# Performance work log

Measured on AMD Instinct MI355X. Metric: run time of the kernel, lower is better.

The kernel has to match this reference:

```python
import jax, jax.numpy as jnp
import numpy as np

H = 16        # num_heads
D = 64        # head_dim
HID = 1024    # hidden_size
WIN = 256     # window_size
GLOBAL = 0    # single global token index {0}


def _rope_tables(L):
    inv_freq = 1.0 / (10000.0 ** (jnp.arange(0, D, 2, dtype=jnp.float32) / D))
    pos = jnp.arange(L, dtype=jnp.float32)
    freqs = pos[:, None] * inv_freq[None, :]          # [L, D/2]
    emb = jnp.concatenate([freqs, freqs], axis=-1)     # [L, D]
    return jnp.cos(emb), jnp.sin(emb)


def _apply_rope(x, cos, sin):
    # x: [B, H, L, D]; cos/sin: [L, D]
    x1, x2 = x[..., : D // 2], x[..., D // 2 :]
    rot = jnp.concatenate([-x2, x1], axis=-1)
    return x * cos[None, None] + rot * sin[None, None]


def setup_inputs() -> dict:
    key = jax.random.key(0)
    ks = jax.random.split(key, 6)
    B, L = 2, 2048
    s = 0.02
    return {
        "hidden_states": jax.random.normal(ks[0], (B, L, HID), jnp.float32),
        "q_w": jax.random.normal(ks[1], (HID, HID), jnp.float32) * s,
        "q_b": jnp.zeros((HID,), jnp.float32),
        "k_w": jax.random.normal(ks[2], (HID, HID), jnp.float32) * s,
        "k_b": jnp.zeros((HID,), jnp.float32),
        "v_w": jax.random.normal(ks[3], (HID, HID), jnp.float32) * s,
        "v_b": jnp.zeros((HID,), jnp.float32),
        "o_w": jax.random.normal(ks[4], (HID, HID), jnp.float32) * s,
        "o_b": jnp.zeros((HID,), jnp.float32),
    }


def reference(hidden_states, q_w, q_b, k_w, k_b, v_w, v_b, o_w, o_b):
    B, L, _ = hidden_states.shape
    # torch Linear: y = x @ W^T + b
    q = hidden_states @ q_w.T + q_b
    k = hidden_states @ k_w.T + k_b
    v = hidden_states @ v_w.T + v_b
    # [B, L, H*D] -> [B, H, L, D]
    q = q.reshape(B, L, H, D).transpose(0, 2, 1, 3)
    k = k.reshape(B, L, H, D).transpose(0, 2, 1, 3)
    v = v.reshape(B, L, H, D).transpose(0, 2, 1, 3)

    cos, sin = _rope_tables(L)
    q = _apply_rope(q, cos, sin)
    k = _apply_rope(k, cos, sin)

    scale = jnp.float32(np.sqrt(D))
    scores = jnp.einsum("bhid,bhjd->bhij", q, k) / scale  # [B, H, L, L]

    # sparse mask: causal AND (within sliding window OR global token)
    i = jnp.arange(L)[:, None]
    j = jnp.arange(L)[None, :]
    keep = (j <= i) & (((i - j) < WIN) | (j == GLOBAL))    # [L, L] bool
    scores = jnp.where(keep[None, None], scores, jnp.float32(-jnp.inf))

    probs = jax.nn.softmax(scores, axis=-1)
    out = jnp.einsum("bhij,bhjd->bhid", probs, v)           # [B, H, L, D]
    out = out.transpose(0, 2, 1, 3).reshape(B, L, HID)
    return out @ o_w.T + o_b
```

## Files before the change

kernel.cpp:

```cpp
#include <hip/hip_runtime.h>
#include <hip/hip_bf16.h>
#include <cstdint>

#define LSEQ   2048
#define HID    1024
#define WIN    256
#define MROWS  4096

typedef unsigned short u16;
typedef unsigned int   u32;
typedef __attribute__((ext_vector_type(8))) short bf16x8;
typedef __attribute__((ext_vector_type(4))) float f32x4;
typedef __attribute__((address_space(1))) const unsigned int as1_uint;
typedef __attribute__((address_space(3))) unsigned int as3_uint;
typedef __attribute__((address_space(3))) char as3_char;

static __device__ __forceinline__ float bf2f(u16 u) {
  union { u32 u; float f; } c; c.u = ((u32)u) << 16; return c.f;
}
static __device__ __forceinline__ u16 f2bf(float f) {
  union { float f; u32 u; } c; c.f = f;
  u32 r = c.u + 0x7fffu + ((c.u >> 16) & 1u);
  return (u16)(r >> 16);
}

__global__ void cvt_all(const float* __restrict__ hidden,
                        const float* __restrict__ qw, const float* __restrict__ kw,
                        const float* __restrict__ vw, const float* __restrict__ ow,
                        u16* __restrict__ hbf, u16* __restrict__ wbf,
                        float* __restrict__ tab) {
  const int b = blockIdx.x;
  if (b >= 8192) {
    const int idx = (b - 8192) * 256 + threadIdx.x;
    const int l = idx >> 5, d = idx & 31;
    float invf = exp2f(-(float)d * (13.287712379549449f / 32.0f));
    float ang = (float)l * invf;
    tab[l * 64 + d]      = cosf(ang);
    tab[l * 64 + 32 + d] = sinf(ang);
    return;
  }
  const int i = b * 256 + threadIdx.x;
  const float* src; u16* dst; int off;
  if (i < (1 << 20)) {
    src = hidden; dst = hbf; off = i;
  } else {
    const int j = i - (1 << 20);
    const int seg = j >> 18;
    off = j & ((1 << 18) - 1);
    src = (seg == 0) ? qw : (seg == 1) ? kw : (seg == 2) ? vw : ow;
    dst = wbf + ((size_t)seg << 20);
  }
  float4 v = ((const float4*)src)[off];
  u32 lo = (u32)f2bf(v.x) | ((u32)f2bf(v.y) << 16);
  u32 hi = (u32)f2bf(v.z) | ((u32)f2bf(v.w) << 16);
  ((uint2*)dst)[off] = make_uint2(lo, hi);
}

template<int NW>
__global__ __launch_bounds__(256, 2) void gemm_bt(
    const u16* __restrict__ A, const u16* __restrict__ W,
    const float* __restrict__ b0, const float* __restrict__ b1, const float* __restrict__ b2,
    u16* __restrict__ outb, float* __restrict__ outf, const float* __restrict__ tab,
    u16* __restrict__ vt)
{
  __shared__ u16 As[128 * 32];
  __shared__ u16 Bs[128 * 32];
  const int tid = threadIdx.x;
  const int lane = tid & 63, w = tid >> 6;
  const int wr = w >> 1, wc = w & 1;

  const int GX = (NW == 3) ? 24 : 8;
  const int CH = (GX * 32) >> 3;
  int fid = blockIdx.y * GX + blockIdx.x;
  fid = (fid & 7) * CH + (fid >> 3);
  const int bx = fid % GX, by = fid / GX;

  const char* gA = (const char*)(A + (size_t)(by*128 + w*32 + (lane >> 2)) * HID) + (lane & 3) * 16;
  const char* gB = (const char*)(W + (size_t)(bx*128 + w*32 + (lane >> 2)) * HID) + (lane & 3) * 16;
  as3_char* lA = (as3_char*)As + w * 2048;
  as3_char* lB = (as3_char*)Bs + w * 2048;

  f32x4 acc[4][4] = {};

  for (int kt = 0; kt < HID; kt += 32) {
    __syncthreads();
    __builtin_amdgcn_global_load_lds((as1_uint*)(gA + kt*2),         (as3_uint*)lA,          16, 0, 0);
    __builtin_amdgcn_global_load_lds((as1_uint*)(gA + kt*2 + 32768), (as3_uint*)(lA + 1024), 16, 0, 0);
    __builtin_amdgcn_global_load_lds((as1_uint*)(gB + kt*2),         (as3_uint*)lB,          16, 0, 0);
    __builtin_amdgcn_global_load_lds((as1_uint*)(gB + kt*2 + 32768), (as3_uint*)(lB + 1024), 16, 0, 0);
    __syncthreads();

    const int kq = (lane >> 4) * 8;
    bf16x8 af[4], bfr[4];
    #pragma unroll
    for (int mm = 0; mm < 4; ++mm)
      af[mm] = *(const bf16x8*)&As[(wr*64 + mm*16 + (lane & 15)) * 32 + kq];
    #pragma unroll
    for (int nn = 0; nn < 4; ++nn)
      bfr[nn] = *(const bf16x8*)&Bs[(wc*64 + nn*16 + (lane & 15)) * 32 + kq];
    #pragma unroll
    for (int mm = 0; mm < 4; ++mm)
      #pragma unroll
      for (int nn = 0; nn < 4; ++nn)
        acc[mm][nn] = __builtin_amdgcn_mfma_f32_16x16x32_bf16(af[mm], bfr[nn], acc[mm][nn], 0, 0, 0);
  }

  const int which = (NW == 3) ? (bx >> 3) : 0;
  const float* bp = (NW == 3) ? (which == 0 ? b0 : (which == 1 ? b1 : b2)) : b0;
  const int cb = (NW == 3) ? ((bx & 7) * 128) : bx * 128;
  u16* ob_ = (NW == 3) ? (outb + (size_t)which * MROWS * HID) : (u16*)nullptr;
  const int rowg = by * 128 + wr * 64;
  const int c = lane & 15, g = lane >> 4;

  #pragma unroll
  for (int nn = 0; nn < 4; ++nn) {
    const float bias = bp[cb + wc * 64 + nn * 16 + c];
    #pragma unroll
    for (int mm = 0; mm < 4; ++mm)
      #pragma unroll
      for (int r = 0; r < 4; ++r) acc[mm][nn][r] += bias;
  }

  if (NW == 3 && which < 2) {
    const float QS = (which == 0) ? (0.125f * 1.4426950408889634f) : 1.0f;
    #pragma unroll
    for (int mm = 0; mm < 4; ++mm) {
      #pragma unroll
      for (int r = 0; r < 4; ++r) {
        const int l = (rowg + mm * 16 + (g << 2) + r) & (LSEQ - 1);
        const float* trow = tab + l * 64;
        const float cs0 = trow[c],      sn0 = trow[32 + c];
        const float cs1 = trow[16 + c], sn1 = trow[48 + c];
        const float x0 = acc[mm][0][r], y0 = acc[mm][2][r];
        const float x1 = acc[mm][1][r], y1 = acc[mm][3][r];
        acc[mm][0][r] = (x0 * cs0 - y0 * sn0) * QS;
        acc[mm][2][r] = (y0 * cs0 + x0 * sn0) * QS;
        acc[mm][1][r] = (x1 * cs1 - y1 * sn1) * QS;
        acc[mm][3][r] = (y1 * cs1 + x1 * sn1) * QS;
      }
    }
  }

  if (NW == 3 && which == 2) {
    #pragma unroll
    for (int nn = 0; nn < 4; ++nn) {
      const int cl = cb + wc * 64 + nn * 16 + c;
      const int hh = cl >> 6, hd = cl & 63;
      #pragma unroll
      for (int mm = 0; mm < 4; ++mm) {
        const int rb = rowg + mm * 16 + (g << 2);
        const int b_ = rb >> 11, l = rb & (LSEQ - 1);
        u16 t4[4];
        #pragma unroll
        for (int r = 0; r < 4; ++r) t4[r] = f2bf(acc[mm][nn][r]);
        *(uint2*)&vt[(size_t)((b_ * 16 + hh) * 64 + hd) * LSEQ + l] = *(uint2*)t4;
      }
    }
  } else {
    #pragma unroll
    for (int nn = 0; nn < 4; ++nn) {
      const int cl = cb + wc * 64 + nn * 16 + c;
      #pragma unroll
      for (int mm = 0; mm < 4; ++mm) {
        const int rb = rowg + mm * 16 + (g << 2);
        #pragma unroll
        for (int r = 0; r < 4; ++r) {
          if (NW == 3) ob_[(size_t)(rb + r) * HID + cl] = f2bf(acc[mm][nn][r]);
          else         outf[(size_t)(rb + r) * HID + cl] = acc[mm][nn][r];
        }
      }
    }
  }
}

__global__ __launch_bounds__(256) void attn_mfma(
    const u16* __restrict__ Q, const u16* __restrict__ K,
    const u16* __restrict__ Vt, u16* __restrict__ O)
{
  __shared__ u16 Ks[2 * 64 * 64];
  __shared__ u16 Vs[2 * 64 * 64];
  __shared__ u16 Ps[4 * 16 * 64];

  const int tid = threadIdx.x, lane = tid & 63, w = tid >> 6;
  const int g = lane >> 4, c = lane & 15;
  const int qb = (blockIdx.x & 31) * 64;
  const int bh = blockIdx.x >> 5;
  const int h = bh & 15;
  const size_t row0 = (size_t)(bh >> 4) * LSEQ;
  const int qw = qb + w * 16;

  const int srow = (w << 4) + (lane >> 3);
  const int scol = ((lane & 7) * 16) ^ ((lane >> 3) << 4);
  const char* gKb = (const char*)(K + (row0 + srow) * HID + h * 64) + scol;
  const char* gVb = (const char*)(Vt + (size_t)(bh * 64 + srow) * LSEQ) + scol;

  const u16* qptr = Q + (row0 + qw + c) * HID + h * 64 + g * 8;
  bf16x8 qa0 = *(const bf16x8*)qptr;
  bf16x8 qa1 = *(const bf16x8*)(qptr + 32);

  const int cbk = qb >> 6;
  int cf = (qb - (WIN - 1)) >> 6; if (cf < 0) cf = 0;

  float psum[4] = {0.f, 0.f, 0.f, 0.f};
  f32x4 o_[4];
  #pragma unroll
  for (int dt = 0; dt < 4; ++dt) o_[dt] = f32x4{0.f, 0.f, 0.f, 0.f};

  if (cf > 0) {
    const u16* k0p = K + row0 * HID + h * 64 + g * 8;
    bf16x8 k0a = *(const bf16x8*)k0p;
    bf16x8 k0b = *(const bf16x8*)(k0p + 32);
    float part = 0.f;
    #pragma unroll
    for (int j = 0; j < 8; ++j)
      part += bf2f((u16)qa0[j]) * bf2f((u16)k0a[j]) + bf2f((u16)qa1[j]) * bf2f((u16)k0b[j]);
    part += __shfl_xor(part, 16);
    part += __shfl_xor(part, 32);
    float p0 = exp2f(part);
    float prs[4];
    #pragma unroll
    for (int r = 0; r < 4; ++r) { prs[r] = __shfl(p0, g * 4 + r); psum[r] = prs[r]; }
    #pragma unroll
    for (int dt = 0; dt < 4; ++dt) {
      float v0 = bf2f(Vt[(size_t)(bh * 64 + dt * 16 + c) * LSEQ]);
      #pragma unroll
      for (int r = 0; r < 4; ++r) o_[dt][r] = prs[r] * v0;
    }
  }

  {
    const size_t kadv = (size_t)cf * 64 * 2048;
    const size_t vadv = (size_t)cf * 128;
    as3_char* lk = (as3_char*)Ks + w * 2048;
    as3_char* lv = (as3_char*)Vs + w * 2048;
    __builtin_amdgcn_global_load_lds((as1_uint*)(gKb + kadv),         (as3_uint*)lk,          16, 0, 0);
    __builtin_amdgcn_global_load_lds((as1_uint*)(gKb + kadv + 16384), (as3_uint*)(lk + 1024), 16, 0, 0);
    __builtin_amdgcn_global_load_lds((as1_uint*)(gVb + vadv),         (as3_uint*)lv,          16, 0, 0);
    __builtin_amdgcn_global_load_lds((as1_uint*)(gVb + vadv + 32768), (as3_uint*)(lv + 1024), 16, 0, 0);
  }

  int buf = 0;
  for (int ci = cf; ci <= cbk; ++ci) {
    const int c0 = ci * 64;
    __syncthreads();

    if (ci < cbk) {
      const size_t kadv = (size_t)(c0 + 64) * 2048;
      const size_t vadv = (size_t)(c0 + 64) * 2;
      as3_char* lk = (as3_char*)Ks + (buf ^ 1) * 8192 + w * 2048;
      as3_char* lv = (as3_char*)Vs + (buf ^ 1) * 8192 + w * 2048;
      __builtin_amdgcn_global_load_lds((as1_uint*)(gKb + kadv),         (as3_uint*)lk,          16, 0, 0);
      __builtin_amdgcn_global_load_lds((as1_uint*)(gKb + kadv + 16384), (as3_uint*)(lk + 1024), 16, 0, 0);
      __builtin_amdgcn_global_load_lds((as1_uint*)(gVb + vadv),         (as3_uint*)lv,          16, 0, 0);
      __builtin_amdgcn_global_load_lds((as1_uint*)(gVb + vadv + 32768), (as3_uint*)(lv + 1024), 16, 0, 0);
    }

    const char* ksbase = (const char*)Ks + buf * 8192;
    const char* vsbase = (const char*)Vs + buf * 8192;

    f32x4 st[4];
    #pragma unroll
    for (int t = 0; t < 4; ++t) {
      const int krow = t * 16 + c;
      const char* kbase = ksbase + krow * 128;
      const int sw = (krow & 7) << 4;
      bf16x8 kb0 = *(const bf16x8*)(kbase + ((g * 16) ^ sw));
      bf16x8 kb1 = *(const bf16x8*)(kbase + ((g * 16 + 64) ^ sw));
      st[t] = f32x4{0.f, 0.f, 0.f, 0.f};
      st[t] = __builtin_amdgcn_mfma_f32_16x16x32_bf16(qa0, kb0, st[t], 0, 0, 0);
      st[t] = __builtin_amdgcn_mfma_f32_16x16x32_bf16(qa1, kb1, st[t], 0, 0, 0);
    }

    float e[4][4];
    #pragma unroll
    for (int r = 0; r < 4; ++r) {
      const int qi = qw + g * 4 + r;
      #pragma unroll
      for (int t = 0; t < 4; ++t) {
        const int kj = c0 + t * 16 + c;
        const bool valid = (kj <= qi) && ((qi - kj < WIN) || (kj == 0));
        e[r][t] = valid ? exp2f(st[t][r]) : 0.f;
      }
      psum[r] += (e[r][0] + e[r][1]) + (e[r][2] + e[r][3]);
    }

    char* pwb = (char*)Ps + w * 2048;
    #pragma unroll
    for (int r = 0; r < 4; ++r) {
      const int q = g * 4 + r;
      char* prow = pwb + q * 128;
      const int sw = (q & 7) << 4;
      *(u16*)(prow + (((c + 0)  * 2) ^ sw)) = f2bf(e[r][0]);
      *(u16*)(prow + (((c + 16) * 2) ^ sw)) = f2bf(e[r][1]);
      *(u16*)(prow + (((c + 32) * 2) ^ sw)) = f2bf(e[r][2]);
      *(u16*)(prow + (((c + 48) * 2) ^ sw)) = f2bf(e[r][3]);
    }
    asm volatile("s_waitcnt lgkmcnt(0)" ::: "memory");
    __builtin_amdgcn_sched_barrier(0);

    bf16x8 pa[2];
    #pragma unroll
    for (int kh = 0; kh < 2; ++kh) {
      const int inner = (g * 16 + kh * 64) ^ ((c & 7) << 4);
      pa[kh] = *(const bf16x8*)(pwb + c * 128 + inner);
    }

    #pragma unroll
    for (int dt = 0; dt < 4; ++dt) {
      const int drow = dt * 16 + c;
      const char* vbase = vsbase + drow * 128;
      const int sw = (drow & 7) << 4;
      bf16x8 vb0 = *(const bf16x8*)(vbase + ((g * 16) ^ sw));
      bf16x8 vb1 = *(const bf16x8*)(vbase + ((g * 16 + 64) ^ sw));
      o_[dt] = __builtin_amdgcn_mfma_f32_16x16x32_bf16(pa[0], vb0, o_[dt], 0, 0, 0);
      o_[dt] = __builtin_amdgcn_mfma_f32_16x16x32_bf16(pa[1], vb1, o_[dt], 0, 0, 0);
    }
    buf ^= 1;
  }

  #pragma unroll
  for (int r = 0; r < 4; ++r) {
    #pragma unroll
    for (int off = 1; off < 16; off <<= 1) psum[r] += __shfl_xor(psum[r], off);
  }

  #pragma unroll
  for (int r = 0; r < 4; ++r) {
    const float inv = 1.f / psum[r];
    u16* orow = O + (row0 + qw + g * 4 + r) * HID + h * 64;
    #pragma unroll
    for (int dt = 0; dt < 4; ++dt)
      orow[dt * 16 + c] = f2bf(o_[dt][r] * inv);
  }
}

extern "C" void kernel_launch(void* const* d_in, const int* in_sizes, int n_in,
                              void* d_out, int out_size, void* d_ws, size_t ws_size,
                              hipStream_t stream) {
  const float* hidden = (const float*)d_in[0];
  const float* qw = (const float*)d_in[1];
  const float* qb = (const float*)d_in[2];
  const float* kw = (const float*)d_in[3];
  const float* kb = (const float*)d_in[4];
  const float* vw = (const float*)d_in[5];
  const float* vb = (const float*)d_in[6];
  const float* ow = (const float*)d_in[7];
  const float* ob = (const float*)d_in[8];
  float* out = (float*)d_out;

  u16* hbf = (u16*)d_ws;
  u16* wbf = hbf + (size_t)MROWS * HID;
  u16* qkv = wbf + (size_t)4 * HID * HID;
  float* tab = (float*)(qkv + (size_t)3 * MROWS * HID);
  u16* Vt = (u16*)(tab + (size_t)LSEQ * 64);

  cvt_all<<<8448, 256, 0, stream>>>(hidden, qw, kw, vw, ow, hbf, wbf, tab);

  gemm_bt<3><<<dim3(24, 32), 256, 0, stream>>>(hbf, wbf, qb, kb, vb, qkv, nullptr, tab, Vt);
  attn_mfma<<<1024, 256, 0, stream>>>(qkv, qkv + (size_t)MROWS * HID, Vt, qkv);
  gemm_bt<1><<<dim3(8, 32), 256, 0, stream>>>(qkv, wbf + (size_t)3 * HID * HID,
                                              ob, ob, ob, nullptr, out, nullptr, nullptr);
}
```

Measured before the change: 93.49 us.

## Double GEMM K-tile to 64 with XOR-swizzled LDS and interleaved RoPE table

The bf16 GEMM now stages K=64 per iteration instead of 32, which halves the number of barrier pairs per K loop. The global-to-LDS layout is rewritten as 128-byte rows with an XOR swizzle, and fragment reads apply the same swizzle to avoid LDS bank conflicts. The RoPE cos/sin table is stored interleaved so the epilogue can fetch each pair with one float2 load. LDS use doubles to 32 KB per block, which may limit occupancy at the requested two blocks per CU.

```diff
diff --git a/kernel.cpp b/kernel.cpp
--- a/kernel.cpp
+++ b/kernel.cpp
@@ -35,8 +35,8 @@
     const int l = idx >> 5, d = idx & 31;
     float invf = exp2f(-(float)d * (13.287712379549449f / 32.0f));
     float ang = (float)l * invf;
-    tab[l * 64 + d]      = cosf(ang);
-    tab[l * 64 + 32 + d] = sinf(ang);
+    tab[l * 64 + 2 * d]     = cosf(ang);
+    tab[l * 64 + 2 * d + 1] = sinf(ang);
     return;
   }
   const int i = b * 256 + threadIdx.x;
@@ -63,11 +63,12 @@
     u16* __restrict__ outb, float* __restrict__ outf, const float* __restrict__ tab,
     u16* __restrict__ vt)
 {
-  __shared__ u16 As[128 * 32];
-  __shared__ u16 Bs[128 * 32];
+  __shared__ u16 As[128 * 64];
+  __shared__ u16 Bs[128 * 64];
   const int tid = threadIdx.x;
   const int lane = tid & 63, w = tid >> 6;
   const int wr = w >> 1, wc = w & 1;
+  const int c = lane & 15, g = lane >> 4;
 
   const int GX = (NW == 3) ? 24 : 8;
   const int CH = (GX * 32) >> 3;
@@ -75,34 +76,45 @@
   fid = (fid & 7) * CH + (fid >> 3);
   const int bx = fid % GX, by = fid / GX;
 
-  const char* gA = (const char*)(A + (size_t)(by*128 + w*32 + (lane >> 2)) * HID) + (lane & 3) * 16;
-  const char* gB = (const char*)(W + (size_t)(bx*128 + w*32 + (lane >> 2)) * HID) + (lane & 3) * 16;
-  as3_char* lA = (as3_char*)As + w * 2048;
-  as3_char* lB = (as3_char*)Bs + w * 2048;
+  const int srow = tid >> 3;
+  const int scolb = ((tid & 7) * 16) ^ ((srow & 7) << 4);
+  const char* gA = (const char*)(A + (size_t)(by * 128 + srow) * HID) + scolb;
+  const char* gB = (const char*)(W + (size_t)(bx * 128 + srow) * HID) + scolb;
 
   f32x4 acc[4][4] = {};
 
-  for (int kt = 0; kt < HID; kt += 32) {
+  for (int kt = 0; kt < HID; kt += 64) {
     __syncthreads();
-    __builtin_amdgcn_global_load_lds((as1_uint*)(gA + kt*2),         (as3_uint*)lA,          16, 0, 0);
-    __builtin_amdgcn_global_load_lds((as1_uint*)(gA + kt*2 + 32768), (as3_uint*)(lA + 1024), 16, 0, 0);
-    __builtin_amdgcn_global_load_lds((as1_uint*)(gB + kt*2),         (as3_uint*)lB,          16, 0, 0);
-    __builtin_amdgcn_global_load_lds((as1_uint*)(gB + kt*2 + 32768), (as3_uint*)(lB + 1024), 16, 0, 0);
+    #pragma unroll
+    for (int r = 0; r < 4; ++r) {
+      __builtin_amdgcn_global_load_lds((as1_uint*)(gA + kt * 2 + r * 32 * (HID * 2)),
+                                       (as3_uint*)((as3_char*)As + r * 4096 + w * 1024), 16, 0, 0);
+      __builtin_amdgcn_global_load_lds((as1_uint*)(gB + kt * 2 + r * 32 * (HID * 2)),
+                                       (as3_uint*)((as3_char*)Bs + r * 4096 + w * 1024), 16, 0, 0);
+    }
     __syncthreads();
 
-    const int kq = (lane >> 4) * 8;
-    bf16x8 af[4], bfr[4];
-    #pragma unroll
-    for (int mm = 0; mm < 4; ++mm)
-      af[mm] = *(const bf16x8*)&As[(wr*64 + mm*16 + (lane & 15)) * 32 + kq];
-    #pragma unroll
-    for (int nn = 0; nn < 4; ++nn)
-      bfr[nn] = *(const bf16x8*)&Bs[(wc*64 + nn*16 + (lane & 15)) * 32 + kq];
-    #pragma unroll
-    for (int mm = 0; mm < 4; ++mm)
-      #pragma unroll
-      for (int nn = 0; nn < 4; ++nn)
-        acc[mm][nn] = __builtin_amdgcn_mfma_f32_16x16x32_bf16(af[mm], bfr[nn], acc[mm][nn], 0, 0, 0);
+    const int sw = (c & 7) << 4;
+    #pragma unroll
+    for (int ks = 0; ks < 2; ++ks) {
+      const int colb = (g * 16 + ks * 64);
+      bf16x8 af[4], bfr[4];
+      #pragma unroll
+      for (int mm = 0; mm < 4; ++mm) {
+        const int row = wr * 64 + mm * 16 + c;
+        af[mm] = *(const bf16x8*)((const char*)As + row * 128 + (colb ^ sw));
+      }
+      #pragma unroll
+      for (int nn = 0; nn < 4; ++nn) {
+        const int row = wc * 64 + nn * 16 + c;
+        bfr[nn] = *(const bf16x8*)((const char*)Bs + row * 128 + (colb ^ sw));
+      }
+      #pragma unroll
+      for (int mm = 0; mm < 4; ++mm)
+        #pragma unroll
+        for (int nn = 0; nn < 4; ++nn)
+          acc[mm][nn] = __builtin_amdgcn_mfma_f32_16x16x32_bf16(af[mm], bfr[nn], acc[mm][nn], 0, 0, 0);
+    }
   }
 
   const int which = (NW == 3) ? (bx >> 3) : 0;
@@ -110,7 +122,6 @@
   const int cb = (NW == 3) ? ((bx & 7) * 128) : bx * 128;
   u16* ob_ = (NW == 3) ? (outb + (size_t)which * MROWS * HID) : (u16*)nullptr;
   const int rowg = by * 128 + wr * 64;
-  const int c = lane & 15, g = lane >> 4;
 
   #pragma unroll
   for (int nn = 0; nn < 4; ++nn) {
@@ -128,15 +139,15 @@
       #pragma unroll
       for (int r = 0; r < 4; ++r) {
         const int l = (rowg + mm * 16 + (g << 2) + r) & (LSEQ - 1);
-        const float* trow = tab + l * 64;
-        const float cs0 = trow[c],      sn0 = trow[32 + c];
-        const float cs1 = trow[16 + c], sn1 = trow[48 + c];
+        const float2* trow = (const float2*)(tab + l * 64);
+        const float2 t0 = trow[c];
+        const float2 t1 = trow[c + 16];
         const float x0 = acc[mm][0][r], y0 = acc[mm][2][r];
         const float x1 = acc[mm][1][r], y1 = acc[mm][3][r];
-        acc[mm][0][r] = (x0 * cs0 - y0 * sn0) * QS;
-        acc[mm][2][r] = (y0 * cs0 + x0 * sn0) * QS;
-        acc[mm][1][r] = (x1 * cs1 - y1 * sn1) * QS;
-        acc[mm][3][r] = (y1 * cs1 + x1 * sn1) * QS;
+        acc[mm][0][r] = (x0 * t0.x - y0 * t0.y) * QS;
+        acc[mm][2][r] = (y0 * t0.x + x0 * t0.y) * QS;
+        acc[mm][1][r] = (x1 * t1.x - y1 * t1.y) * QS;
+        acc[mm][3][r] = (y1 * t1.x + x1 * t1.y) * QS;
       }
     }
   }
```

Result: faster. 89.52 us, median of 2 (-4.2%).
